# Performance work log

Hardware: AMD Instinct MI355X
Metric: run time of the kernel (lower is better)

Reference implementation:

```python
import jax, jax.numpy as jnp
import numpy as np

MAXLEN = 100  # target_node_incoming_edge_maxlim in to_dense_batch_JY


def setup_inputs() -> dict:
    key = jax.random.key(0)
    ks = jax.random.split(key, 6)
    N, F, H, B = 500000, 64, 64, 8192
    x = jax.random.normal(ks[0], (N, F), dtype=jnp.float32)
    index = jnp.sort(jax.random.randint(ks[1], (N,), 0, B)).astype(jnp.int64)
    s = 1.0 / np.sqrt(H)  # torch LSTM reset_parameters: U(-1/sqrt(H), 1/sqrt(H))
    W_ih = jax.random.uniform(ks[2], (4 * H, F), jnp.float32, -s, s)
    W_hh = jax.random.uniform(ks[3], (4 * H, H), jnp.float32, -s, s)
    b_ih = jax.random.uniform(ks[4], (4 * H,), jnp.float32, -s, s)
    b_hh = jax.random.uniform(ks[5], (4 * H,), jnp.float32, -s, s)
    return {"x": x, "W_ih": W_ih, "W_hh": W_hh, "b_ih": b_ih, "b_hh": b_hh,
            "index": index, "dim_size": B}


def _lstm_last_hidden(dense, mask, W_ih, W_hh, b_ih, b_hh):
    """Run a single-layer LSTM over dense [B,L,F]; freeze state where mask is
    False, which reproduces pack_sequence semantics (ht = hidden at last valid
    step of each sequence; zero-length sequences stay at h0=0)."""
    B, L, F = dense.shape
    H = W_hh.shape[1]
    # input projection for all timesteps at once: [B, L, 4H]
    xg = jnp.einsum('blf,gf->blg', dense, W_ih) + (b_ih + b_hh)

    def step(carry, inp):
        h, c = carry
        g_x, m = inp                      # g_x: [B,4H], m: [B] bool
        g = g_x + h @ W_hh.T
        i, f, gc, o = jnp.split(g, 4, axis=-1)  # torch gate order: i, f, g, o
        i = jax.nn.sigmoid(i)
        f = jax.nn.sigmoid(f)
        gc = jnp.tanh(gc)
        o = jax.nn.sigmoid(o)
        c_new = f * c + i * gc
        h_new = o * jnp.tanh(c_new)
        m2 = m[:, None]
        return (jnp.where(m2, h_new, h), jnp.where(m2, c_new, c)), None

    h0 = jnp.zeros((B, H), dense.dtype)
    (h, _c), _ = jax.lax.scan(step, (h0, h0),
                              (jnp.swapaxes(xg, 0, 1), mask.T))
    return h  # [B, H] == ht[-1]


def reference(x, W_ih, W_hh, b_ih, b_hh, index, dim_size):
    N, F = x.shape
    index = index.astype(jnp.int32)
    # per-graph node counts and exclusive-cumsum offsets (index is sorted)
    counts = jax.ops.segment_sum(jnp.ones(N, jnp.int32), index,
                                 num_segments=dim_size)
    offsets = jnp.concatenate([jnp.zeros(1, jnp.int32),
                               jnp.cumsum(counts)[:-1].astype(jnp.int32)])
    pos = jnp.arange(N, dtype=jnp.int32) - offsets[index]  # position in graph
    valid = pos < MAXLEN                                   # truncate to 100
    # scatter into dense [B, MAXLEN, F]; invalid rows are zeroed and added at
    # slot 0 so they are no-ops
    dense = jnp.zeros((dim_size, MAXLEN, F), x.dtype)
    dense = dense.at[index, jnp.where(valid, pos, 0)].add(
        jnp.where(valid[:, None], x, 0.0))
    seq_len = jnp.minimum(counts, MAXLEN)
    mask = jnp.arange(MAXLEN)[None, :] < seq_len[:, None]  # [B, MAXLEN]
    return _lstm_last_hidden(dense, mask, W_ih, W_hh, b_ih, b_hh)
```

## Files before the change

kernel.cpp:

```cpp
#include <hip/hip_runtime.h>

#define MAXLEN 100
#define HDIM 64
#define CH 4
#define NSEG 16
#define SROW 72
#define SPLANE (CH * SROW + 8)
#define HSTR 72
#define L2E 1.44269504f

typedef __attribute__((ext_vector_type(8))) short bf16x8;
typedef __attribute__((ext_vector_type(4))) float f32x4;

#define LGKM_BARRIER() asm volatile("s_waitcnt lgkmcnt(0)\n\ts_barrier" ::: "memory")

__device__ __forceinline__ unsigned cvtpk(float a, float b) {
    unsigned r;
    asm("v_cvt_pk_bf16_f32 %0, %1, %2" : "=v"(r) : "v"(a), "v"(b));
    return r;
}
__device__ __forceinline__ bf16x8 pack8(f32x4 a, f32x4 b) {
    union { unsigned u[4]; bf16x8 v; } c;
    c.u[0] = cvtpk(a[0], a[1]); c.u[1] = cvtpk(a[2], a[3]);
    c.u[2] = cvtpk(b[0], b[1]); c.u[3] = cvtpk(b[2], b[3]);
    return c.v;
}
__device__ __forceinline__ float sig_pre(float a) {
    return __builtin_amdgcn_rcpf(1.0f + __builtin_amdgcn_exp2f(a));
}
__device__ __forceinline__ float tanh_pre(float a) {
    return fmaf(2.0f, __builtin_amdgcn_rcpf(1.0f + __builtin_amdgcn_exp2f(a)), -1.0f);
}
__device__ __forceinline__ float tanh_p(float v) {
    return fmaf(2.0f, __builtin_amdgcn_rcpf(1.0f + __builtin_amdgcn_exp2f(v * (-2.0f * L2E))), -1.0f);
}

__global__ void seg_bounds_kernel(const int* __restrict__ index,
                                  int* __restrict__ segStart, int N, int B) {
    const int s = blockIdx.x * blockDim.x + threadIdx.x;
    if (s > B) return;
    int lo = 0, hi = N;
    while (lo < hi) { int m = (lo + hi) >> 1; if (index[m] < s) lo = m + 1; else hi = m; }
    segStart[s] = lo;
}

__global__ __launch_bounds__(1024)
void seg_sort_kernel(const int* __restrict__ segStart,
                     int2* __restrict__ slotPacked, int B, int nslots) {
    __shared__ int hist_s[MAXLEN + 1], base_s[MAXLEN + 1], cnt_s[MAXLEN + 1];
    const int tid = threadIdx.x;
    if (tid <= MAXLEN) { hist_s[tid] = 0; cnt_s[tid] = 0; }
    __syncthreads();
    int myS0[8], myLen[8];
#pragma unroll
    for (int j = 0; j < 8; ++j) {
        const int s = tid + j * 1024;
        myS0[j] = 0; myLen[j] = -1;
        if (s < B) {
            const int a = segStart[s];
            int len = segStart[s + 1] - a;
            len = len < MAXLEN ? len : MAXLEN;
            myS0[j] = a; myLen[j] = len;
            atomicAdd(&hist_s[len], 1);
        }
    }
    __syncthreads();
    if (tid == 0) {
        int acc = 0;
        for (int l = MAXLEN; l >= 0; --l) { base_s[l] = acc; acc += hist_s[l]; }
    }
    __syncthreads();
#pragma unroll
    for (int j = 0; j < 8; ++j) {
        if (myLen[j] >= 0) {
            const int s = tid + j * 1024;
            const int slot = base_s[myLen[j]] + atomicAdd(&cnt_s[myLen[j]], 1);
            slotPacked[slot] = make_int2(myS0[j], (s << 7) | myLen[j]);
        }
    }
    if (tid < nslots - B) slotPacked[B + tid] = make_int2(0, -128);
}

__global__ __launch_bounds__(256, 2)
void lstm16_kernel(const float* __restrict__ x,
                   const float* __restrict__ Wih,
                   const float* __restrict__ Whh,
                   const float* __restrict__ bih,
                   const float* __restrict__ bhh,
                   const int* __restrict__ index,
                   const int2* __restrict__ slotPacked,
                   float* __restrict__ out, int N, int B) {
    const int tid  = threadIdx.x;
    const int w    = tid >> 6;
    const int lane = tid & 63;
    const int l15  = lane & 15;
    const int quad = lane >> 4;
    const int segbase = blockIdx.x * NSEG;
    const int ncol = w * 16 + l15;

    __shared__ __align__(16) unsigned short xst[NSEG * SPLANE];
    __shared__ __align__(16) unsigned short hst[2][16][HSTR];
    __shared__ int sstart[NSEG], slen[NSEG], sseg[NSEG];

    if (tid < NSEG) {
        const int slot = segbase + tid;
        int sg = -1, s = 0, len = 0;
        if (slotPacked != nullptr) {
            const int2 p = slotPacked[slot];
            s   = p.x;
            sg  = p.y >> 7;
            len = p.y & 127;
        } else {
            const int b = slot;
            if (b < B) {
                sg = b;
                int lo = 0, hi = N;
                while (lo < hi) { int m = (lo + hi) >> 1; if (index[m] < b) lo = m + 1; else hi = m; }
                s = lo;
                hi = N;
                while (lo < hi) { int m = (lo + hi) >> 1; if (index[m] < b + 1) lo = m + 1; else hi = m; }
                len = lo - s;
                len = len < MAXLEN ? len : MAXLEN;
            }
        }
        sstart[tid] = s;
        slen[tid] = len;
        sseg[tid] = sg;
    }
    for (int i = tid; i < 2 * 16 * HSTR / 2; i += 256) ((int*)hst)[i] = 0;
    __syncthreads();

    bf16x8 wi[4][2], wh[4][2];
    f32x4 bsv[4];
#pragma unroll
    for (int g = 0; g < 4; ++g) {
        const float sc = (g == 2) ? (-2.0f * L2E) : (-L2E);
        const int row = g * HDIM + ncol;
        const float bb = sc * (bih[row] + bhh[row]);
        bsv[g][0] = bb; bsv[g][1] = bb; bsv[g][2] = bb; bsv[g][3] = bb;
#pragma unroll
        for (int kt = 0; kt < 2; ++kt) {
            const f32x4* pi = (const f32x4*)(Wih + (size_t)row * HDIM + kt * 32 + quad * 8);
            const f32x4* ph = (const f32x4*)(Whh + (size_t)row * HDIM + kt * 32 + quad * 8);
            wi[g][kt] = pack8(pi[0] * sc, pi[1] * sc);
            wh[g][kt] = pack8(ph[0] * sc, ph[1] * sc);
        }
    }

    int len4[4];
#pragma unroll
    for (int r = 0; r < 4; ++r) len4[r] = slen[quad * 4 + r];
    int lmax = 0;
#pragma unroll
    for (int i = 0; i < NSEG; ++i) { int v = slen[i]; lmax = v > lmax ? v : lmax; }
    lmax = __builtin_amdgcn_readfirstlane(lmax);

    const int sS = tid >> 4, sT = (tid >> 2) & 3, sC = tid & 3;
    const int sst = sstart[sS];
    const int sln = slen[sS];

    f32x4 pre[4];

#define ISSUE(t0_)                                                              \
    {                                                                           \
        int ct = (t0_) + sT;                                                    \
        ct = (sln > 0) ? (ct < sln ? ct : sln - 1) : 0;                         \
        int row = sst + ct;                                                     \
        row = row < N - 1 ? row : N - 1;                                        \
        const f32x4* p_ = (const f32x4*)(x + (size_t)row * HDIM + sC * 16);     \
        pre[0] = p_[0]; pre[1] = p_[1]; pre[2] = p_[2]; pre[3] = p_[3];         \
    }
#define COMMIT()                                                                \
    {                                                                           \
        uint4 o1, o2;                                                           \
        o1.x = cvtpk(pre[0][0], pre[0][1]); o1.y = cvtpk(pre[0][2], pre[0][3]); \
        o1.z = cvtpk(pre[1][0], pre[1][1]); o1.w = cvtpk(pre[1][2], pre[1][3]); \
        o2.x = cvtpk(pre[2][0], pre[2][1]); o2.y = cvtpk(pre[2][2], pre[2][3]); \
        o2.z = cvtpk(pre[3][0], pre[3][1]); o2.w = cvtpk(pre[3][2], pre[3][3]); \
        unsigned short* d_ = &xst[sS * SPLANE + sT * SROW + sC * 16];           \
        *(uint4*)d_ = o1; *(uint4*)(d_ + 8) = o2;                               \
    }

    const unsigned short* xb = &xst[l15 * SPLANE + quad * 8];

    f32x4 accx[4];
#define ACCX(tt_)                                                               \
    {                                                                           \
        const unsigned short* xr_ = xb + (tt_) * SROW;                          \
        bf16x8 xa0_ = *(const bf16x8*)(xr_);                                    \
        bf16x8 xa1_ = *(const bf16x8*)(xr_ + 32);                               \
        _Pragma("unroll")                                                       \
        for (int g_ = 0; g_ < 4; ++g_) {                                        \
            f32x4 a_ = __builtin_amdgcn_mfma_f32_16x16x32_bf16(xa0_, wi[g_][0], bsv[g_], 0, 0, 0); \
            accx[g_] = __builtin_amdgcn_mfma_f32_16x16x32_bf16(xa1_, wi[g_][1], a_, 0, 0, 0); \
        }                                                                       \
    }

    float c4[4] = {0, 0, 0, 0}, h4[4] = {0, 0, 0, 0};
    const int nch = (lmax + CH - 1) / CH;

    if (nch > 0) {
        ISSUE(0);
        COMMIT();
        LGKM_BARRIER();
        ACCX(0);
        if (nch > 1) ISSUE(CH);

        for (int ch = 0; ch < nch; ++ch) {
            const int t0 = ch * CH;
#pragma unroll
            for (int tt = 0; tt < CH; ++tt) {
                const int t = t0 + tt;
                const int pb = tt & 1, nb = pb ^ 1;

                const unsigned short* hr = &hst[pb][l15][quad * 8];
                bf16x8 ha0 = *(const bf16x8*)(hr);
                bf16x8 ha1 = *(const bf16x8*)(hr + 32);

                f32x4 acc[4];
#pragma unroll
                for (int g = 0; g < 4; ++g) {
                    f32x4 a = __builtin_amdgcn_mfma_f32_16x16x32_bf16(ha0, wh[g][0], accx[g], 0, 0, 0);
                    acc[g] = __builtin_amdgcn_mfma_f32_16x16x32_bf16(ha1, wh[g][1], a, 0, 0, 0);
                }

                if (tt + 1 < CH) ACCX(tt + 1);

#pragma unroll
                for (int r = 0; r < 4; ++r) {
                    float gi = sig_pre (acc[0][r]);
                    float gf = sig_pre (acc[1][r]);
                    float gg = tanh_pre(acc[2][r]);
                    float go = sig_pre (acc[3][r]);
                    float cn = fmaf(gf, c4[r], gi * gg);
                    float hn = go * tanh_p(cn);
                    const bool up = t < len4[r];
                    c4[r] = up ? cn : c4[r];
                    h4[r] = up ? hn : h4[r];
                    hst[nb][quad * 4 + r][ncol] = (unsigned short)cvtpk(h4[r], h4[r]);
                }
                LGKM_BARRIER();
            }
            if (ch + 1 < nch) {
                COMMIT();
                LGKM_BARRIER();
                ACCX(0);
                if (ch + 2 < nch) ISSUE((ch + 2) * CH);
            }
        }
    }

#pragma unroll
    for (int r = 0; r < 4; ++r) {
        const int sg = sseg[quad * 4 + r];
        if (sg >= 0) out[(size_t)sg * HDIM + ncol] = h4[r];
    }
#undef ISSUE
#undef COMMIT
#undef ACCX
}

extern "C" void kernel_launch(void* const* d_in, const int* in_sizes, int n_in,
                              void* d_out, int out_size, void* d_ws, size_t ws_size,
                              hipStream_t stream) {
    const float* x   = (const float*)d_in[0];
    const float* Wih = (const float*)d_in[1];
    const float* Whh = (const float*)d_in[2];
    const float* bih = (const float*)d_in[3];
    const float* bhh = (const float*)d_in[4];
    const int* index = (const int*)d_in[5];

    const int N = in_sizes[5];
    const int B = out_size / HDIM;
    const int nblocks = (B + NSEG - 1) / NSEG;
    const int nslots = nblocks * NSEG;

    int slotOfs = (B + 1 + 7) & ~7;
    const size_t need = ((size_t)slotOfs + 2 * (size_t)nslots) * sizeof(int);
    const bool sortOK = (d_ws != nullptr) && (ws_size >= need) && (B <= 8192);

    if (sortOK) {
        int* segStart = (int*)d_ws;
        int2* slotPacked = (int2*)((int*)d_ws + slotOfs);
        const int k1blocks = (B + 1 + 255) / 256;
        seg_bounds_kernel<<<k1blocks, 256, 0, stream>>>(index, segStart, N, B);
        seg_sort_kernel<<<1, 1024, 0, stream>>>(segStart, slotPacked, B, nslots);
        lstm16_kernel<<<nblocks, 256, 0, stream>>>(x, Wih, Whh, bih, bhh, index,
                                                   slotPacked, (float*)d_out, N, B);
    } else {
        lstm16_kernel<<<nblocks, 256, 0, stream>>>(x, Wih, Whh, bih, bhh, index,
                                                   nullptr, (float*)d_out, N, B);
    }
}
```

Before: 232.4 us.

## Halve segments per block to double block count and raise occupancy

Reduces segments per workgroup from 16 to 8, duplicating each segment across two MFMA rows and using only half the waves for x staging. This doubles the number of blocks and raises launch bounds to 4 blocks per CU, so more independent recurrences run at once to hide the latency of the serial LSTM step chain. In exchange, half of the MFMA work is redundant, and tighter register limits could cause spills. The hidden-state LDS row stride also changes, which alters the bank-conflict pattern.

Result: slower. 284.8 us (+22.6%).

```diff
diff --git a/kernel.cpp b/kernel.cpp
--- a/kernel.cpp
+++ b/kernel.cpp
@@ -3,10 +3,10 @@
 #define MAXLEN 100
 #define HDIM 64
 #define CH 4
-#define NSEG 16
+#define NSEG 8
 #define SROW 72
 #define SPLANE (CH * SROW + 8)
-#define HSTR 72
+#define HSTR 80
 #define L2E 1.44269504f
 
 typedef __attribute__((ext_vector_type(8))) short bf16x8;
@@ -81,15 +81,15 @@
     if (tid < nslots - B) slotPacked[B + tid] = make_int2(0, -128);
 }
 
-__global__ __launch_bounds__(256, 2)
-void lstm16_kernel(const float* __restrict__ x,
-                   const float* __restrict__ Wih,
-                   const float* __restrict__ Whh,
-                   const float* __restrict__ bih,
-                   const float* __restrict__ bhh,
-                   const int* __restrict__ index,
-                   const int2* __restrict__ slotPacked,
-                   float* __restrict__ out, int N, int B) {
+__global__ __launch_bounds__(256, 4)
+void lstm8_kernel(const float* __restrict__ x,
+                  const float* __restrict__ Wih,
+                  const float* __restrict__ Whh,
+                  const float* __restrict__ bih,
+                  const float* __restrict__ bhh,
+                  const int* __restrict__ index,
+                  const int2* __restrict__ slotPacked,
+                  float* __restrict__ out, int N, int B) {
     const int tid  = threadIdx.x;
     const int w    = tid >> 6;
     const int lane = tid & 63;
@@ -99,7 +99,7 @@
     const int ncol = w * 16 + l15;
 
     __shared__ __align__(16) unsigned short xst[NSEG * SPLANE];
-    __shared__ __align__(16) unsigned short hst[2][16][HSTR];
+    __shared__ __align__(16) unsigned short hst[2][NSEG][HSTR];
     __shared__ int sstart[NSEG], slen[NSEG], sseg[NSEG];
 
     if (tid < NSEG) {
@@ -127,7 +127,7 @@
         slen[tid] = len;
         sseg[tid] = sg;
     }
-    for (int i = tid; i < 2 * 16 * HSTR / 2; i += 256) ((int*)hst)[i] = 0;
+    for (int i = tid; i < 2 * NSEG * HSTR / 2; i += 256) ((int*)hst)[i] = 0;
     __syncthreads();
 
     bf16x8 wi[4][2], wh[4][2];
@@ -147,22 +147,22 @@
         }
     }
 
-    int len4[4];
-#pragma unroll
-    for (int r = 0; r < 4; ++r) len4[r] = slen[quad * 4 + r];
+    int len2[2];
+#pragma unroll
+    for (int j = 0; j < 2; ++j) len2[j] = slen[quad * 2 + j];
     int lmax = 0;
 #pragma unroll
     for (int i = 0; i < NSEG; ++i) { int v = slen[i]; lmax = v > lmax ? v : lmax; }
     lmax = __builtin_amdgcn_readfirstlane(lmax);
 
     const int sS = tid >> 4, sT = (tid >> 2) & 3, sC = tid & 3;
-    const int sst = sstart[sS];
-    const int sln = slen[sS];
+    const int sst = (tid < 128) ? sstart[sS] : 0;
+    const int sln = (tid < 128) ? slen[sS] : 0;
 
     f32x4 pre[4];
 
 #define ISSUE(t0_)                                                              \
-    {                                                                           \
+    if (w < 2) {                                                                \
         int ct = (t0_) + sT;                                                    \
         ct = (sln > 0) ? (ct < sln ? ct : sln - 1) : 0;                         \
         int row = sst + ct;                                                     \
@@ -171,7 +171,7 @@
         pre[0] = p_[0]; pre[1] = p_[1]; pre[2] = p_[2]; pre[3] = p_[3];         \
     }
 #define COMMIT()                                                                \
-    {                                                                           \
+    if (w < 2) {                                                                \
         uint4 o1, o2;                                                           \
         o1.x = cvtpk(pre[0][0], pre[0][1]); o1.y = cvtpk(pre[0][2], pre[0][3]); \
         o1.z = cvtpk(pre[1][0], pre[1][1]); o1.w = cvtpk(pre[1][2], pre[1][3]); \
@@ -181,7 +181,7 @@
         *(uint4*)d_ = o1; *(uint4*)(d_ + 8) = o2;                               \
     }
 
-    const unsigned short* xb = &xst[l15 * SPLANE + quad * 8];
+    const unsigned short* xb = &xst[(l15 >> 1) * SPLANE + quad * 8];
 
     f32x4 accx[4];
 #define ACCX(tt_)                                                               \
@@ -196,7 +196,7 @@
         }                                                                       \
     }
 
-    float c4[4] = {0, 0, 0, 0}, h4[4] = {0, 0, 0, 0};
+    float c2[2] = {0, 0}, h2[2] = {0, 0};
     const int nch = (lmax + CH - 1) / CH;
 
     if (nch > 0) {
@@ -213,7 +213,7 @@
                 const int t = t0 + tt;
                 const int pb = tt & 1, nb = pb ^ 1;
 
-                const unsigned short* hr = &hst[pb][l15][quad * 8];
+                const unsigned short* hr = &hst[pb][l15 >> 1][quad * 8];
                 bf16x8 ha0 = *(const bf16x8*)(hr);
                 bf16x8 ha1 = *(const bf16x8*)(hr + 32);
 
@@ -227,17 +227,18 @@
                 if (tt + 1 < CH) ACCX(tt + 1);
 
 #pragma unroll
-                for (int r = 0; r < 4; ++r) {
+                for (int j = 0; j < 2; ++j) {
+                    const int r = 2 * j;
                     float gi = sig_pre (acc[0][r]);
                     float gf = sig_pre (acc[1][r]);
                     float gg = tanh_pre(acc[2][r]);
                     float go = sig_pre (acc[3][r]);
-                    float cn = fmaf(gf, c4[r], gi * gg);
+                    float cn = fmaf(gf, c2[j], gi * gg);
                     float hn = go * tanh_p(cn);
-                    const bool up = t < len4[r];
-                    c4[r] = up ? cn : c4[r];
-                    h4[r] = up ? hn : h4[r];
-                    hst[nb][quad * 4 + r][ncol] = (unsigned short)cvtpk(h4[r], h4[r]);
+                    const bool up = t < len2[j];
+                    c2[j] = up ? cn : c2[j];
+                    h2[j] = up ? hn : h2[j];
+                    hst[nb][quad * 2 + j][ncol] = (unsigned short)cvtpk(h2[j], h2[j]);
                 }
                 LGKM_BARRIER();
             }
@@ -251,9 +252,9 @@
     }
 
 #pragma unroll
-    for (int r = 0; r < 4; ++r) {
-        const int sg = sseg[quad * 4 + r];
-        if (sg >= 0) out[(size_t)sg * HDIM + ncol] = h4[r];
+    for (int j = 0; j < 2; ++j) {
+        const int sg = sseg[quad * 2 + j];
+        if (sg >= 0) out[(size_t)sg * HDIM + ncol] = h2[j];
     }
 #undef ISSUE
 #undef COMMIT
@@ -285,10 +286,10 @@
         const int k1blocks = (B + 1 + 255) / 256;
         seg_bounds_kernel<<<k1blocks, 256, 0, stream>>>(index, segStart, N, B);
         seg_sort_kernel<<<1, 1024, 0, stream>>>(segStart, slotPacked, B, nslots);
-        lstm16_kernel<<<nblocks, 256, 0, stream>>>(x, Wih, Whh, bih, bhh, index,
-                                                   slotPacked, (float*)d_out, N, B);
+        lstm8_kernel<<<nblocks, 256, 0, stream>>>(x, Wih, Whh, bih, bhh, index,
+                                                  slotPacked, (float*)d_out, N, B);
     } else {
-        lstm16_kernel<<<nblocks, 256, 0, stream>>>(x, Wih, Whh, bih, bhh, index,
-                                                   nullptr, (float*)d_out, N, B);
-    }
-}
+        lstm8_kernel<<<nblocks, 256, 0, stream>>>(x, Wih, Whh, bih, bhh, index,
+                                                  nullptr, (float*)d_out, N, B);
+    }
+}
```
